# Performance work log

Hardware: AMD Instinct MI355X
Metric: run time of the kernel (lower is better)

Reference implementation:

```python
import jax, jax.numpy as jnp
import numpy as np

B, DIM, C, TOPK = 2, 256, 19, 256
GAMMA = 0.999
HF, WF = 128, 128   # feature spatial res
H, W = 512, 512     # label spatial res
EPS = 1e-12         # F.normalize eps


def setup_inputs() -> dict:
    key = jax.random.key(0)
    k1, k2, k3, k4, k5 = jax.random.split(key, 5)
    features = jax.random.normal(k1, (B, DIM, HF, WF), jnp.float32)
    weight = jax.random.uniform(k2, (B, C, HF, WF), jnp.float32)
    prototypes = jax.random.normal(k3, (C, DIM), jnp.float32)
    update_count = jax.random.randint(k4, (C,), 0, 3).astype(jnp.float32)
    labels = jax.random.randint(k5, (B, H, W), 0, C).astype(jnp.int32)
    return {"features": features, "weight": weight, "prototypes": prototypes,
            "update_count": update_count, "labels": labels}


def _l2norm(x):
    return x / jnp.maximum(jnp.linalg.norm(x, axis=-1, keepdims=True), EPS)


def reference(features, weight, prototypes, update_count, labels):
    # bilinear resize to label resolution (align_corners=False semantics)
    feats = jax.image.resize(features, (B, DIM, H, W), "bilinear")
    wt = jax.image.resize(weight, (B, C, H, W), "bilinear")
    feats = feats.transpose(0, 2, 3, 1).reshape(-1, DIM)   # [N, D]
    wt = wt.transpose(0, 2, 3, 1).reshape(-1, C)           # [N, C]
    lab = labels.reshape(-1)                               # [N]
    valid = lab != 255
    # per-class pixel mask; weights are >=0 (softmax-like), so zeroing
    # out-of-class pixels is equivalent to the torch masked top-k
    cls_mask = valid[:, None] & (lab[:, None] == jnp.arange(C)[None, :])  # [N,C]
    w_cls = jnp.where(cls_mask, wt, 0.0)                   # [N, C]
    topw, topi = jax.lax.top_k(w_cls.T, TOPK)              # [C, K]
    wsum = topw.sum(-1)                                    # [C]
    top_feats = feats[topi]                                # [C, K, D]
    proto = jnp.einsum('ck,ckd->cd', topw, top_feats) / jnp.maximum(wsum, EPS)[:, None]
    proto = _l2norm(proto)                                 # F.normalize before EMA
    has = cls_mask.any(0) & (wsum > 0)                     # class present with nonzero weight
    gamma = jnp.where(update_count == 0, 0.0,
                      jnp.minimum(1.0 - 1.0 / (update_count + 1.0), GAMMA))
    new = gamma[:, None] * prototypes + (1.0 - gamma)[:, None] * proto
    new = jnp.where(has[:, None], new, prototypes)
    new_count = update_count + has.astype(update_count.dtype)
    new = _l2norm(new)                                     # final global normalize
    return new, new_count
```

## Files before the change

kernel.cpp:

```cpp
#include <hip/hip_runtime.h>

#define NB 2
#define NC 19
#define ND 256
#define HFDIM 128
#define SRC_HW 16384
#define HOUT 512
#define NPIX (NB*HOUT*HOUT)
#define KTOP 256
#define NBUCK 16384
#define CAPC 1024
#define CAPE 24
#define NCHUNK 512
#define CHPX 64
#define NBK2 128
#define NDCAP 24
#define NCCAP 24
#define NSLICE 8
#define EPSF 1e-12f

#define AL(x) (((x)+255)&~(size_t)255)
static constexpr size_t OFF_PART  = 0;
static constexpr size_t SZ_PART   = (size_t)NCHUNK*NC*ND*4;
static constexpr size_t OFF_HIST  = 0;
static constexpr size_t OFF_WKEYS = AL(OFF_HIST + (size_t)NC*NBUCK*4);
static constexpr size_t OFF_DLIST = AL(OFF_WKEYS + (size_t)NPIX*4);
static constexpr size_t OFF_CLIST = AL(OFF_DLIST + (size_t)NC*NBK2*NDCAP*8);
static constexpr size_t ALIAS_END = OFF_CLIST + (size_t)NC*NBK2*NCCAP*8;
static_assert(ALIAS_END <= SZ_PART, "alias overflow");
static constexpr size_t OFF_DCNT  = AL(OFF_PART + SZ_PART);
static constexpr size_t OFF_CCNT  = OFF_DCNT + (size_t)NC*NBK2*4;
static constexpr size_t OFF_ECNT  = OFF_CCNT + (size_t)NC*NBK2*4;
static constexpr size_t ZERO_BEG  = OFF_DCNT;
static constexpr size_t ZERO_SZ   = OFF_ECNT + (size_t)NCHUNK*NC*4 - ZERO_BEG;
static constexpr size_t OFF_CUT16 = AL(OFF_ECNT + (size_t)NCHUNK*NC*4);
static constexpr size_t OFF_NHI   = OFF_CUT16 + 256;
static constexpr size_t OFF_CNT   = OFF_NHI   + 256;
static constexpr size_t OFF_WSUM  = OFF_CNT   + 256;
static constexpr size_t OFF_EDATA = AL(OFF_WSUM + 256);
static constexpr size_t OFF_PART2 = AL(OFF_EDATA + (size_t)NCHUNK*NC*CAPE*8);
static constexpr size_t WS_NEED   = OFF_PART2 + (size_t)NSLICE*NC*ND*4;

__device__ __forceinline__ unsigned hperm(unsigned b) { return (b * 5651u) & (NBUCK-1); }

__device__ __forceinline__ void tap1d(int o, int& i0, int& i1, float& f) {
  float pos = (float)o * 0.25f - 0.375f;
  int t0 = (int)floorf(pos);
  float ff = pos - (float)t0;
  int a = t0, b = t0 + 1;
  if (t0 < 0)           { a = 0;       b = 0;       ff = 0.f; }
  else if (b > HFDIM-1) { b = HFDIM-1; ff = 0.f; }
  i0 = a; i1 = b; f = ff;
}

__global__ __launch_bounds__(256) void k_keys(const float* __restrict__ weight,
                                              const int* __restrict__ labels,
                                              float* __restrict__ wkeys,
                                              unsigned* __restrict__ hist) {
  int i4 = blockIdx.x * 256 + threadIdx.x;
  int4 lab = ((const int4*)labels)[i4];
  int n0 = i4 * 4;
  int b = n0 >> 18, y = (n0 >> 9) & 511, x0 = n0 & 511;
  int ya, yb; float fy;
  tap1d(y, ya, yb, fy);
  int labs[4] = {lab.x, lab.y, lab.z, lab.w};
  float wv[4];
  #pragma unroll
  for (int j = 0; j < 4; ++j) {
    int l = labs[j]; float w = 0.f;
    if (l >= 0 && l < NC) {
      int xa, xb; float fx; tap1d(x0 + j, xa, xb, fx);
      const float* pl = weight + (((size_t)(b*NC + l)) << 14);
      float v00 = pl[ya*HFDIM+xa], v10 = pl[yb*HFDIM+xa];
      float v01 = pl[ya*HFDIM+xb], v11 = pl[yb*HFDIM+xb];
      float cA = fmaf(fy, v10, (1.f-fy)*v00);
      float cB = fmaf(fy, v11, (1.f-fy)*v01);
      w = fmaf(fx, cB, (1.f-fx)*cA);
      unsigned bk = __float_as_uint(w) >> 16;
      if (bk > NBUCK-1) bk = NBUCK-1;
      atomicAdd(&hist[l*NBUCK + hperm(bk)], 1u);
    }
    wv[j] = w;
  }
  ((float4*)wkeys)[i4] = make_float4(wv[0], wv[1], wv[2], wv[3]);
}

__global__ __launch_bounds__(256) void k_sel1(const unsigned* __restrict__ hist,
                                              unsigned* __restrict__ cut16,
                                              unsigned* __restrict__ nhi,
                                              unsigned* __restrict__ cnttot) {
  int c = blockIdx.x, t = threadIdx.x;
  __shared__ unsigned sfx[256];
  __shared__ unsigned vals[64];
  __shared__ int sChunk;
  const unsigned* h = hist + (size_t)c * NBUCK;
  unsigned s = 0;
  for (int i = 0; i < 64; ++i) s += h[hperm((unsigned)(t*64 + i))];
  sfx[t] = s;
  if (t == 0) sChunk = -1;
  __syncthreads();
  for (int off = 1; off < 256; off <<= 1) {
    unsigned u = (t + off < 256) ? sfx[t + off] : 0;
    __syncthreads();
    sfx[t] += u;
    __syncthreads();
  }
  unsigned total = sfx[0];
  if (t == 0) cnttot[c] = total;
  unsigned mysfx = sfx[t];
  unsigned nxt = (t < 255) ? sfx[t + 1] : 0;
  if (mysfx >= KTOP && nxt < KTOP) sChunk = t;
  __syncthreads();
  int chunk = sChunk;
  if (chunk < 0) {
    if (t == 0) { cut16[c] = 0; nhi[c] = total - h[hperm(0u)]; }
    return;
  }
  unsigned nAbove = (chunk < 255) ? sfx[chunk + 1] : 0;
  if (t < 64) vals[t] = h[hperm((unsigned)(chunk*64 + t))];
  __syncthreads();
  for (int off = 1; off < 64; off <<= 1) {
    unsigned u = 0;
    if (t < 64) u = (t + off < 64) ? vals[t + off] : 0;
    __syncthreads();
    if (t < 64) vals[t] += u;
    __syncthreads();
  }
  if (t < 64) {
    unsigned sv  = vals[t] + nAbove;
    unsigned svn = (t < 63) ? vals[t + 1] + nAbove : nAbove;
    if (sv >= KTOP && svn < KTOP) { cut16[c] = (unsigned)(chunk*64 + t); nhi[c] = svn; }
  }
}

__global__ __launch_bounds__(256) void k_compact(const int* __restrict__ labels,
                                                 const float* __restrict__ wkeys,
                                                 const unsigned* __restrict__ cut16,
                                                 unsigned* __restrict__ dcnt2, uint2* __restrict__ dlist2,
                                                 unsigned* __restrict__ ccnt2, uint2* __restrict__ clist2) {
  __shared__ unsigned scut[NC], lcnt[NC], lcnt2[NC];
  int t = threadIdx.x, blk = blockIdx.x;
  if (t < NC) { scut[t] = cut16[t]; lcnt[t] = 0; lcnt2[t] = 0; }
  __syncthreads();
  int i4base = blk * 1024;
  for (int it = 0; it < 4; ++it) {
    int i4 = i4base + it*256 + t;
    int4 lab = ((const int4*)labels)[i4];
    float4 wv = ((const float4*)wkeys)[i4];
    int n0 = i4 * 4;
    int labs[4] = {lab.x, lab.y, lab.z, lab.w};
    float ws_[4] = {wv.x, wv.y, wv.z, wv.w};
    #pragma unroll
    for (int j = 0; j < 4; ++j) {
      int l = labs[j]; if (l < 0 || l >= NC) continue;
      unsigned key = __float_as_uint(ws_[j]);
      unsigned pre = key >> 16, cc = scut[l];
      if (pre > cc) {
        unsigned s = atomicAdd(&lcnt[l], 1u);
        if (s < NDCAP) dlist2[((size_t)l*NBK2 + blk)*NDCAP + s] = make_uint2(key, (unsigned)(n0 + j));
      } else if (pre == cc) {
        unsigned s = atomicAdd(&lcnt2[l], 1u);
        if (s < NCCAP) clist2[((size_t)l*NBK2 + blk)*NCCAP + s] = make_uint2(key, (unsigned)(n0 + j));
      }
    }
  }
  __syncthreads();
  if (t < NC) {
    dcnt2[t*NBK2 + blk] = min(lcnt[t],  (unsigned)NDCAP);
    ccnt2[t*NBK2 + blk] = min(lcnt2[t], (unsigned)NCCAP);
  }
}

__device__ __forceinline__ void emit(int c, int sp, float coef,
                                     unsigned* ecnt, uint2* edata) {
  if (coef == 0.f) return;
  int chunk = sp >> 6, pl = sp & 63;
  unsigned s = atomicAdd(&ecnt[chunk*NC + c], 1u);
  if (s < CAPE) edata[((size_t)(chunk*NC + c))*CAPE + s] = make_uint2((unsigned)pl, __float_as_uint(coef));
}

__device__ __forceinline__ void append_taps(int c, unsigned pix, float w,
                                            unsigned* ecnt, uint2* edata) {
  int n = (int)pix; int b = n >> 18, y = (n >> 9) & 511, x = n & 511;
  int ya, yb, xa, xb; float fy, fx;
  tap1d(y, ya, yb, fy); tap1d(x, xa, xb, fx);
  float c00 = (1.f-fy)*(1.f-fx)*w, c01 = (1.f-fy)*fx*w;
  float c10 = fy*(1.f-fx)*w,       c11 = fy*fx*w;
  int base = b * SRC_HW;
  emit(c, base + ya*HFDIM + xa, c00, ecnt, edata);
  emit(c, base + ya*HFDIM + xb, c01, ecnt, edata);
  emit(c, base + yb*HFDIM + xa, c10, ecnt, edata);
  emit(c, base + yb*HFDIM + xb, c11, ecnt, edata);
}

__global__ __launch_bounds__(256) void k_sel3(const uint2* __restrict__ dlist2, const unsigned* __restrict__ dcnt2,
                                              const uint2* __restrict__ clist2, const unsigned* __restrict__ ccnt2,
                                              const unsigned* __restrict__ cut16, const unsigned* __restrict__ nhi,
                                              unsigned* __restrict__ ecnt, uint2* __restrict__ edata,
                                              float* __restrict__ wsum) {
  int c = blockIdx.x, t = threadIdx.x;
  __shared__ uint2 dl[KTOP];
  __shared__ uint2 cand[CAPC];
  __shared__ unsigned ps[256], hh[256];
  __shared__ unsigned sPfx; __shared__ int sNeed; __shared__ unsigned sTie;
  __shared__ float red[256];

  unsigned cnt = (t < NBK2) ? dcnt2[c*NBK2 + t] : 0;
  ps[t] = cnt;
  __syncthreads();
  for (int off = 1; off < 256; off <<= 1) {
    unsigned v = (t >= off) ? ps[t - off] : 0;
    __syncthreads();
    ps[t] += v;
    __syncthreads();
  }
  int dn = (int)ps[255];
  unsigned base = ps[t] - cnt;
  if (t < NBK2) for (unsigned i = 0; i < cnt; ++i) {
    if (base + i < KTOP) dl[base + i] = dlist2[((size_t)c*NBK2 + t)*NDCAP + i];
  }
  __syncthreads();
  unsigned cnt2 = (t < NBK2) ? ccnt2[c*NBK2 + t] : 0;
  ps[t] = cnt2;
  __syncthreads();
  for (int off = 1; off < 256; off <<= 1) {
    unsigned v = (t >= off) ? ps[t - off] : 0;
    __syncthreads();
    ps[t] += v;
    __syncthreads();
  }
  int m = (int)ps[255];
  unsigned base2 = ps[t] - cnt2;
  if (t < NBK2) for (unsigned i = 0; i < cnt2; ++i) {
    if (base2 + i < CAPC) cand[base2 + i] = clist2[((size_t)c*NBK2 + t)*NCCAP + i];
  }
  if (m > CAPC) m = CAPC;
  if (dn > KTOP) dn = KTOP;
  if (t == 0) { sPfx = cut16[c] << 16; sNeed = KTOP - (int)nhi[c]; sTie = 0; }
  __syncthreads();
  for (int rnd = 0; rnd < 2; ++rnd) {
    int sh = rnd ? 0 : 8;
    hh[t] = 0;
    __syncthreads();
    unsigned hiMask = ~((1u << (sh + 8)) - 1u);
    unsigned pfx = sPfx; int need = sNeed;
    for (int k = t; k < m; k += 256) {
      unsigned key = cand[k].x;
      if ((key & hiMask) == (pfx & hiMask)) atomicAdd(&hh[(key >> sh) & 255u], 1u);
    }
    __syncthreads();
    for (int off = 1; off < 256; off <<= 1) {
      unsigned u = (t + off < 256) ? hh[t + off] : 0;
      __syncthreads();
      hh[t] += u;
      __syncthreads();
    }
    unsigned sv = hh[t], svn = (t < 255) ? hh[t + 1] : 0;
    if ((int)sv >= need && (int)svn < need) { sPfx = pfx | ((unsigned)t << sh); sNeed = need - (int)svn; }
    if (t == 0 && (int)hh[0] < need)        { sPfx = pfx; sNeed = need - (int)hh[1]; }
    __syncthreads();
  }
  unsigned cutkey = sPfx;
  int needeq = max(sNeed, 0);
  __syncthreads();
  float wacc = 0.f;
  for (int k = t; k < dn; k += 256) {
    uint2 e = dl[k];
    float w = __uint_as_float(e.x);
    wacc += w;
    append_taps(c, e.y, w, ecnt, edata);
  }
  for (int k = t; k < m; k += 256) {
    uint2 e = cand[k];
    bool sel = e.x > cutkey;
    if (!sel && e.x == cutkey) sel = (atomicAdd(&sTie, 1u) < (unsigned)needeq);
    if (sel) {
      float w = __uint_as_float(e.x);
      wacc += w;
      append_taps(c, e.y, w, ecnt, edata);
    }
  }
  red[t] = wacc; __syncthreads();
  for (int s = 128; s > 0; s >>= 1) { if (t < s) red[t] += red[t + s]; __syncthreads(); }
  if (t == 0) wsum[c] = red[0];
}

__global__ __launch_bounds__(256) void k_contract(const float* __restrict__ feat,
                                                  const unsigned* __restrict__ ecnt,
                                                  const uint2* __restrict__ edata,
                                                  float* __restrict__ part) {
  __shared__ float tile[CHPX * 256];
  int chunk = blockIdx.x, t = threadIdx.x;
  int b = chunk >> 8;
  int p0 = (chunk & 255) << 6;
  const float4* fp = (const float4*)(feat + (((size_t)(b*ND + t)) << 14) + p0);
  #pragma unroll
  for (int i = 0; i < 16; ++i) {
    float4 v = fp[i];
    int p = i * 4;
    tile[(p+0)*256 + t] = v.x; tile[(p+1)*256 + t] = v.y;
    tile[(p+2)*256 + t] = v.z; tile[(p+3)*256 + t] = v.w;
  }
  __syncthreads();
  float* outp = part + ((size_t)chunk * NC) * ND + t;
  #pragma unroll
  for (int c = 0; c < NC; ++c) {
    int n = min((int)ecnt[chunk*NC + c], CAPE);
    const uint2* ed = edata + ((size_t)(chunk*NC + c)) * CAPE;
    float acc = 0.f;
    for (int e = 0; e < n; ++e) {
      uint2 u = ed[e];
      acc = fmaf(__uint_as_float(u.y), tile[u.x*256 + t], acc);
    }
    outp[(size_t)c * ND] = acc;
  }
}

__global__ __launch_bounds__(256) void k_reduce(const float* __restrict__ part,
                                                float* __restrict__ part2) {
  int s = blockIdx.x & (NSLICE-1);
  int c = blockIdx.x / NSLICE;
  int d = threadIdx.x;
  const float* p = part + ((size_t)(s * (NCHUNK/NSLICE)) * NC + c) * ND + d;
  float acc = 0.f;
  #pragma unroll 8
  for (int r = 0; r < NCHUNK/NSLICE; ++r) acc += p[(size_t)r * NC * ND];
  part2[((size_t)s * NC + c) * ND + d] = acc;
}

__global__ __launch_bounds__(256) void k_final(const float* __restrict__ part2,
                                               const float* __restrict__ wsum,
                                               const unsigned* __restrict__ cnttot,
                                               const float* __restrict__ protos,
                                               const float* __restrict__ ucount,
                                               float* __restrict__ out) {
  int c = blockIdx.x, d = threadIdx.x;
  __shared__ float red[256];
  const float* p2 = part2 + (size_t)c * ND + d;
  float psum = 0.f;
  #pragma unroll
  for (int s = 0; s < NSLICE; ++s) psum += p2[(size_t)s * NC * ND];
  float ws = wsum[c];
  float proto = psum / fmaxf(ws, EPSF);
  red[d] = proto * proto;
  __syncthreads();
  for (int s = 128; s > 0; s >>= 1) { if (d < s) red[d] += red[d + s]; __syncthreads(); }
  float norm1 = sqrtf(red[0]);
  __syncthreads();
  float pn = proto / fmaxf(norm1, EPSF);
  float uc = ucount[c];
  float gamma = (uc == 0.f) ? 0.f : fminf(1.f - 1.f / (uc + 1.f), 0.999f);
  bool has = (cnttot[c] > 0u) && (ws > 0.f);
  float oldv = protos[c * ND + d];
  float nv = has ? fmaf(gamma, oldv, (1.f - gamma) * pn) : oldv;
  red[d] = nv * nv;
  __syncthreads();
  for (int s = 128; s > 0; s >>= 1) { if (d < s) red[d] += red[d + s]; __syncthreads(); }
  float norm2 = sqrtf(red[0]);
  out[c * ND + d] = nv / fmaxf(norm2, EPSF);
  if (d == 0) out[NC * ND + c] = uc + (has ? 1.f : 0.f);
}

extern "C" void kernel_launch(void* const* d_in, const int* in_sizes, int n_in,
                              void* d_out, int out_size, void* d_ws, size_t ws_size,
                              hipStream_t stream) {
  const float* feat   = (const float*)d_in[0];
  const float* weight = (const float*)d_in[1];
  const float* protos = (const float*)d_in[2];
  const float* ucount = (const float*)d_in[3];
  const int*   labels = (const int*)d_in[4];
  float* out = (float*)d_out;
  if (ws_size < WS_NEED) return;

  char* ws = (char*)d_ws;
  unsigned* hist   = (unsigned*)(ws + OFF_HIST);
  float*    wkeys  = (float*)   (ws + OFF_WKEYS);
  uint2*    dlist2 = (uint2*)   (ws + OFF_DLIST);
  uint2*    clist2 = (uint2*)   (ws + OFF_CLIST);
  float*    part   = (float*)   (ws + OFF_PART);
  unsigned* dcnt2  = (unsigned*)(ws + OFF_DCNT);
  unsigned* ccnt2  = (unsigned*)(ws + OFF_CCNT);
  unsigned* ecnt   = (unsigned*)(ws + OFF_ECNT);
  unsigned* cut16  = (unsigned*)(ws + OFF_CUT16);
  unsigned* nhiB   = (unsigned*)(ws + OFF_NHI);
  unsigned* cnttot = (unsigned*)(ws + OFF_CNT);
  float*    wsum   = (float*)   (ws + OFF_WSUM);
  uint2*    edata  = (uint2*)   (ws + OFF_EDATA);
  float*    part2  = (float*)   (ws + OFF_PART2);

  hipMemsetAsync(ws + OFF_HIST, 0, (size_t)NC*NBUCK*4, stream);
  hipMemsetAsync(ws + ZERO_BEG, 0, ZERO_SZ, stream);
  k_keys    <<<NPIX/1024, 256, 0, stream>>>(weight, labels, wkeys, hist);
  k_sel1    <<<NC,        256, 0, stream>>>(hist, cut16, nhiB, cnttot);
  k_compact <<<NBK2,      256, 0, stream>>>(labels, wkeys, cut16, dcnt2, dlist2, ccnt2, clist2);
  k_sel3    <<<NC,        256, 0, stream>>>(dlist2, dcnt2, clist2, ccnt2, cut16, nhiB, ecnt, edata, wsum);
  k_contract<<<NCHUNK,    256, 0, stream>>>(feat, ecnt, edata, part);
  k_reduce  <<<NC*NSLICE, 256, 0, stream>>>(part, part2);
  k_final   <<<NC,        256, 0, stream>>>(part2, wsum, cnttot, protos, ucount, out);
}
```

Baseline: 162.8 us.

## Fuse all pipeline stages into one cooperative persistent kernel with grid syncs

Replaces the two memsets and seven separate kernel launches with a single cooperative kernel of 256 blocks. Stages are separated by grid.sync, and shared memory is reused across stages through a union. The aim is to remove per-launch overhead and inter-kernel gaps. In exchange, the grid-wide barriers cost time, the large streaming stages now run on fewer blocks via grid-stride loops, and the 64KB shared union limits occupancy for every stage.

```diff
diff --git a/kernel.cpp b/kernel.cpp
--- a/kernel.cpp
+++ b/kernel.cpp
@@ -1,4 +1,6 @@
 #include <hip/hip_runtime.h>
+#include <hip/hip_cooperative_groups.h>
+namespace cg = cooperative_groups;
 
 #define NB 2
 #define NC 19
@@ -17,6 +19,7 @@
 #define NDCAP 24
 #define NCCAP 24
 #define NSLICE 8
+#define NGRID 256
 #define EPSF 1e-12f
 
 #define AL(x) (((x)+255)&~(size_t)255)
@@ -32,7 +35,7 @@
 static constexpr size_t OFF_CCNT  = OFF_DCNT + (size_t)NC*NBK2*4;
 static constexpr size_t OFF_ECNT  = OFF_CCNT + (size_t)NC*NBK2*4;
 static constexpr size_t ZERO_BEG  = OFF_DCNT;
-static constexpr size_t ZERO_SZ   = OFF_ECNT + (size_t)NCHUNK*NC*4 - ZERO_BEG;
+static constexpr size_t ZCNT      = (2*(size_t)NC*NBK2*4 + (size_t)NCHUNK*NC*4) / 4;
 static constexpr size_t OFF_CUT16 = AL(OFF_ECNT + (size_t)NCHUNK*NC*4);
 static constexpr size_t OFF_NHI   = OFF_CUT16 + 256;
 static constexpr size_t OFF_CNT   = OFF_NHI   + 256;
@@ -51,124 +54,6 @@
   if (t0 < 0)           { a = 0;       b = 0;       ff = 0.f; }
   else if (b > HFDIM-1) { b = HFDIM-1; ff = 0.f; }
   i0 = a; i1 = b; f = ff;
-}
-
-__global__ __launch_bounds__(256) void k_keys(const float* __restrict__ weight,
-                                              const int* __restrict__ labels,
-                                              float* __restrict__ wkeys,
-                                              unsigned* __restrict__ hist) {
-  int i4 = blockIdx.x * 256 + threadIdx.x;
-  int4 lab = ((const int4*)labels)[i4];
-  int n0 = i4 * 4;
-  int b = n0 >> 18, y = (n0 >> 9) & 511, x0 = n0 & 511;
-  int ya, yb; float fy;
-  tap1d(y, ya, yb, fy);
-  int labs[4] = {lab.x, lab.y, lab.z, lab.w};
-  float wv[4];
-  #pragma unroll
-  for (int j = 0; j < 4; ++j) {
-    int l = labs[j]; float w = 0.f;
-    if (l >= 0 && l < NC) {
-      int xa, xb; float fx; tap1d(x0 + j, xa, xb, fx);
-      const float* pl = weight + (((size_t)(b*NC + l)) << 14);
-      float v00 = pl[ya*HFDIM+xa], v10 = pl[yb*HFDIM+xa];
-      float v01 = pl[ya*HFDIM+xb], v11 = pl[yb*HFDIM+xb];
-      float cA = fmaf(fy, v10, (1.f-fy)*v00);
-      float cB = fmaf(fy, v11, (1.f-fy)*v01);
-      w = fmaf(fx, cB, (1.f-fx)*cA);
-      unsigned bk = __float_as_uint(w) >> 16;
-      if (bk > NBUCK-1) bk = NBUCK-1;
-      atomicAdd(&hist[l*NBUCK + hperm(bk)], 1u);
-    }
-    wv[j] = w;
-  }
-  ((float4*)wkeys)[i4] = make_float4(wv[0], wv[1], wv[2], wv[3]);
-}
-
-__global__ __launch_bounds__(256) void k_sel1(const unsigned* __restrict__ hist,
-                                              unsigned* __restrict__ cut16,
-                                              unsigned* __restrict__ nhi,
-                                              unsigned* __restrict__ cnttot) {
-  int c = blockIdx.x, t = threadIdx.x;
-  __shared__ unsigned sfx[256];
-  __shared__ unsigned vals[64];
-  __shared__ int sChunk;
-  const unsigned* h = hist + (size_t)c * NBUCK;
-  unsigned s = 0;
-  for (int i = 0; i < 64; ++i) s += h[hperm((unsigned)(t*64 + i))];
-  sfx[t] = s;
-  if (t == 0) sChunk = -1;
-  __syncthreads();
-  for (int off = 1; off < 256; off <<= 1) {
-    unsigned u = (t + off < 256) ? sfx[t + off] : 0;
-    __syncthreads();
-    sfx[t] += u;
-    __syncthreads();
-  }
-  unsigned total = sfx[0];
-  if (t == 0) cnttot[c] = total;
-  unsigned mysfx = sfx[t];
-  unsigned nxt = (t < 255) ? sfx[t + 1] : 0;
-  if (mysfx >= KTOP && nxt < KTOP) sChunk = t;
-  __syncthreads();
-  int chunk = sChunk;
-  if (chunk < 0) {
-    if (t == 0) { cut16[c] = 0; nhi[c] = total - h[hperm(0u)]; }
-    return;
-  }
-  unsigned nAbove = (chunk < 255) ? sfx[chunk + 1] : 0;
-  if (t < 64) vals[t] = h[hperm((unsigned)(chunk*64 + t))];
-  __syncthreads();
-  for (int off = 1; off < 64; off <<= 1) {
-    unsigned u = 0;
-    if (t < 64) u = (t + off < 64) ? vals[t + off] : 0;
-    __syncthreads();
-    if (t < 64) vals[t] += u;
-    __syncthreads();
-  }
-  if (t < 64) {
-    unsigned sv  = vals[t] + nAbove;
-    unsigned svn = (t < 63) ? vals[t + 1] + nAbove : nAbove;
-    if (sv >= KTOP && svn < KTOP) { cut16[c] = (unsigned)(chunk*64 + t); nhi[c] = svn; }
-  }
-}
-
-__global__ __launch_bounds__(256) void k_compact(const int* __restrict__ labels,
-                                                 const float* __restrict__ wkeys,
-                                                 const unsigned* __restrict__ cut16,
-                                                 unsigned* __restrict__ dcnt2, uint2* __restrict__ dlist2,
-                                                 unsigned* __restrict__ ccnt2, uint2* __restrict__ clist2) {
-  __shared__ unsigned scut[NC], lcnt[NC], lcnt2[NC];
-  int t = threadIdx.x, blk = blockIdx.x;
-  if (t < NC) { scut[t] = cut16[t]; lcnt[t] = 0; lcnt2[t] = 0; }
-  __syncthreads();
-  int i4base = blk * 1024;
-  for (int it = 0; it < 4; ++it) {
-    int i4 = i4base + it*256 + t;
-    int4 lab = ((const int4*)labels)[i4];
-    float4 wv = ((const float4*)wkeys)[i4];
-    int n0 = i4 * 4;
-    int labs[4] = {lab.x, lab.y, lab.z, lab.w};
-    float ws_[4] = {wv.x, wv.y, wv.z, wv.w};
-    #pragma unroll
-    for (int j = 0; j < 4; ++j) {
-      int l = labs[j]; if (l < 0 || l >= NC) continue;
-      unsigned key = __float_as_uint(ws_[j]);
-      unsigned pre = key >> 16, cc = scut[l];
-      if (pre > cc) {
-        unsigned s = atomicAdd(&lcnt[l], 1u);
-        if (s < NDCAP) dlist2[((size_t)l*NBK2 + blk)*NDCAP + s] = make_uint2(key, (unsigned)(n0 + j));
-      } else if (pre == cc) {
-        unsigned s = atomicAdd(&lcnt2[l], 1u);
-        if (s < NCCAP) clist2[((size_t)l*NBK2 + blk)*NCCAP + s] = make_uint2(key, (unsigned)(n0 + j));
-      }
-    }
-  }
-  __syncthreads();
-  if (t < NC) {
-    dcnt2[t*NBK2 + blk] = min(lcnt[t],  (unsigned)NDCAP);
-    ccnt2[t*NBK2 + blk] = min(lcnt2[t], (unsigned)NCCAP);
-  }
 }
 
 __device__ __forceinline__ void emit(int c, int sp, float coef,
@@ -193,172 +78,314 @@
   emit(c, base + yb*HFDIM + xb, c11, ecnt, edata);
 }
 
-__global__ __launch_bounds__(256) void k_sel3(const uint2* __restrict__ dlist2, const unsigned* __restrict__ dcnt2,
-                                              const uint2* __restrict__ clist2, const unsigned* __restrict__ ccnt2,
-                                              const unsigned* __restrict__ cut16, const unsigned* __restrict__ nhi,
-                                              unsigned* __restrict__ ecnt, uint2* __restrict__ edata,
-                                              float* __restrict__ wsum) {
-  int c = blockIdx.x, t = threadIdx.x;
-  __shared__ uint2 dl[KTOP];
-  __shared__ uint2 cand[CAPC];
-  __shared__ unsigned ps[256], hh[256];
-  __shared__ unsigned sPfx; __shared__ int sNeed; __shared__ unsigned sTie;
-  __shared__ float red[256];
-
-  unsigned cnt = (t < NBK2) ? dcnt2[c*NBK2 + t] : 0;
-  ps[t] = cnt;
-  __syncthreads();
-  for (int off = 1; off < 256; off <<= 1) {
-    unsigned v = (t >= off) ? ps[t - off] : 0;
-    __syncthreads();
-    ps[t] += v;
-    __syncthreads();
-  }
-  int dn = (int)ps[255];
-  unsigned base = ps[t] - cnt;
-  if (t < NBK2) for (unsigned i = 0; i < cnt; ++i) {
-    if (base + i < KTOP) dl[base + i] = dlist2[((size_t)c*NBK2 + t)*NDCAP + i];
-  }
-  __syncthreads();
-  unsigned cnt2 = (t < NBK2) ? ccnt2[c*NBK2 + t] : 0;
-  ps[t] = cnt2;
-  __syncthreads();
-  for (int off = 1; off < 256; off <<= 1) {
-    unsigned v = (t >= off) ? ps[t - off] : 0;
-    __syncthreads();
-    ps[t] += v;
-    __syncthreads();
-  }
-  int m = (int)ps[255];
-  unsigned base2 = ps[t] - cnt2;
-  if (t < NBK2) for (unsigned i = 0; i < cnt2; ++i) {
-    if (base2 + i < CAPC) cand[base2 + i] = clist2[((size_t)c*NBK2 + t)*NCCAP + i];
-  }
-  if (m > CAPC) m = CAPC;
-  if (dn > KTOP) dn = KTOP;
-  if (t == 0) { sPfx = cut16[c] << 16; sNeed = KTOP - (int)nhi[c]; sTie = 0; }
-  __syncthreads();
-  for (int rnd = 0; rnd < 2; ++rnd) {
-    int sh = rnd ? 0 : 8;
-    hh[t] = 0;
-    __syncthreads();
-    unsigned hiMask = ~((1u << (sh + 8)) - 1u);
-    unsigned pfx = sPfx; int need = sNeed;
-    for (int k = t; k < m; k += 256) {
-      unsigned key = cand[k].x;
-      if ((key & hiMask) == (pfx & hiMask)) atomicAdd(&hh[(key >> sh) & 255u], 1u);
-    }
-    __syncthreads();
-    for (int off = 1; off < 256; off <<= 1) {
-      unsigned u = (t + off < 256) ? hh[t + off] : 0;
-      __syncthreads();
-      hh[t] += u;
-      __syncthreads();
-    }
-    unsigned sv = hh[t], svn = (t < 255) ? hh[t + 1] : 0;
-    if ((int)sv >= need && (int)svn < need) { sPfx = pfx | ((unsigned)t << sh); sNeed = need - (int)svn; }
-    if (t == 0 && (int)hh[0] < need)        { sPfx = pfx; sNeed = need - (int)hh[1]; }
-    __syncthreads();
-  }
-  unsigned cutkey = sPfx;
-  int needeq = max(sNeed, 0);
-  __syncthreads();
-  float wacc = 0.f;
-  for (int k = t; k < dn; k += 256) {
-    uint2 e = dl[k];
-    float w = __uint_as_float(e.x);
-    wacc += w;
-    append_taps(c, e.y, w, ecnt, edata);
-  }
-  for (int k = t; k < m; k += 256) {
-    uint2 e = cand[k];
-    bool sel = e.x > cutkey;
-    if (!sel && e.x == cutkey) sel = (atomicAdd(&sTie, 1u) < (unsigned)needeq);
-    if (sel) {
-      float w = __uint_as_float(e.x);
-      wacc += w;
-      append_taps(c, e.y, w, ecnt, edata);
-    }
-  }
-  red[t] = wacc; __syncthreads();
-  for (int s = 128; s > 0; s >>= 1) { if (t < s) red[t] += red[t + s]; __syncthreads(); }
-  if (t == 0) wsum[c] = red[0];
-}
-
-__global__ __launch_bounds__(256) void k_contract(const float* __restrict__ feat,
-                                                  const unsigned* __restrict__ ecnt,
-                                                  const uint2* __restrict__ edata,
-                                                  float* __restrict__ part) {
-  __shared__ float tile[CHPX * 256];
-  int chunk = blockIdx.x, t = threadIdx.x;
-  int b = chunk >> 8;
-  int p0 = (chunk & 255) << 6;
-  const float4* fp = (const float4*)(feat + (((size_t)(b*ND + t)) << 14) + p0);
-  #pragma unroll
-  for (int i = 0; i < 16; ++i) {
-    float4 v = fp[i];
-    int p = i * 4;
-    tile[(p+0)*256 + t] = v.x; tile[(p+1)*256 + t] = v.y;
-    tile[(p+2)*256 + t] = v.z; tile[(p+3)*256 + t] = v.w;
-  }
-  __syncthreads();
-  float* outp = part + ((size_t)chunk * NC) * ND + t;
-  #pragma unroll
-  for (int c = 0; c < NC; ++c) {
-    int n = min((int)ecnt[chunk*NC + c], CAPE);
-    const uint2* ed = edata + ((size_t)(chunk*NC + c)) * CAPE;
-    float acc = 0.f;
-    for (int e = 0; e < n; ++e) {
-      uint2 u = ed[e];
-      acc = fmaf(__uint_as_float(u.y), tile[u.x*256 + t], acc);
-    }
-    outp[(size_t)c * ND] = acc;
-  }
-}
-
-__global__ __launch_bounds__(256) void k_reduce(const float* __restrict__ part,
-                                                float* __restrict__ part2) {
-  int s = blockIdx.x & (NSLICE-1);
-  int c = blockIdx.x / NSLICE;
-  int d = threadIdx.x;
-  const float* p = part + ((size_t)(s * (NCHUNK/NSLICE)) * NC + c) * ND + d;
-  float acc = 0.f;
-  #pragma unroll 8
-  for (int r = 0; r < NCHUNK/NSLICE; ++r) acc += p[(size_t)r * NC * ND];
-  part2[((size_t)s * NC + c) * ND + d] = acc;
-}
-
-__global__ __launch_bounds__(256) void k_final(const float* __restrict__ part2,
-                                               const float* __restrict__ wsum,
-                                               const unsigned* __restrict__ cnttot,
+__global__ __launch_bounds__(256) void k_fused(const float* __restrict__ feat,
+                                               const float* __restrict__ weight,
                                                const float* __restrict__ protos,
                                                const float* __restrict__ ucount,
-                                               float* __restrict__ out) {
-  int c = blockIdx.x, d = threadIdx.x;
-  __shared__ float red[256];
-  const float* p2 = part2 + (size_t)c * ND + d;
-  float psum = 0.f;
-  #pragma unroll
-  for (int s = 0; s < NSLICE; ++s) psum += p2[(size_t)s * NC * ND];
-  float ws = wsum[c];
-  float proto = psum / fmaxf(ws, EPSF);
-  red[d] = proto * proto;
-  __syncthreads();
-  for (int s = 128; s > 0; s >>= 1) { if (d < s) red[d] += red[d + s]; __syncthreads(); }
-  float norm1 = sqrtf(red[0]);
-  __syncthreads();
-  float pn = proto / fmaxf(norm1, EPSF);
-  float uc = ucount[c];
-  float gamma = (uc == 0.f) ? 0.f : fminf(1.f - 1.f / (uc + 1.f), 0.999f);
-  bool has = (cnttot[c] > 0u) && (ws > 0.f);
-  float oldv = protos[c * ND + d];
-  float nv = has ? fmaf(gamma, oldv, (1.f - gamma) * pn) : oldv;
-  red[d] = nv * nv;
-  __syncthreads();
-  for (int s = 128; s > 0; s >>= 1) { if (d < s) red[d] += red[d + s]; __syncthreads(); }
-  float norm2 = sqrtf(red[0]);
-  out[c * ND + d] = nv / fmaxf(norm2, EPSF);
-  if (d == 0) out[NC * ND + c] = uc + (has ? 1.f : 0.f);
+                                               const int* __restrict__ labels,
+                                               float* __restrict__ out,
+                                               char* __restrict__ ws) {
+  cg::grid_group grid = cg::this_grid();
+  const int tid = threadIdx.x, bid = blockIdx.x, gdim = gridDim.x;
+  const int gthreads = gdim * 256;
+
+  unsigned* hist   = (unsigned*)(ws + OFF_HIST);
+  float*    wkeys  = (float*)   (ws + OFF_WKEYS);
+  uint2*    dlist2 = (uint2*)   (ws + OFF_DLIST);
+  uint2*    clist2 = (uint2*)   (ws + OFF_CLIST);
+  float*    part   = (float*)   (ws + OFF_PART);
+  unsigned* dcnt2  = (unsigned*)(ws + OFF_DCNT);
+  unsigned* ccnt2  = (unsigned*)(ws + OFF_CCNT);
+  unsigned* ecnt   = (unsigned*)(ws + OFF_ECNT);
+  unsigned* cut16  = (unsigned*)(ws + OFF_CUT16);
+  unsigned* nhi    = (unsigned*)(ws + OFF_NHI);
+  unsigned* cnttot = (unsigned*)(ws + OFF_CNT);
+  float*    wsum   = (float*)   (ws + OFF_WSUM);
+  uint2*    edata  = (uint2*)   (ws + OFF_EDATA);
+  float*    part2  = (float*)   (ws + OFF_PART2);
+
+  __shared__ union {
+    float tile[CHPX * 256];
+    struct { unsigned sfx[256]; unsigned vals[64]; int sChunk; } s1;
+    struct { unsigned scut[NC], lcnt[NC], lcnt2[NC]; } s3;
+    struct {
+      unsigned dlk[KTOP], dlp[KTOP];
+      unsigned ck[CAPC], cp[CAPC];
+      unsigned ps[256], hh[256];
+      unsigned sPfx; int sNeed; unsigned sTie;
+      float red[256];
+    } s4;
+    float redf[256];
+  } sh;
+
+  const int gtid = bid * 256 + tid;
+
+  for (unsigned i = gtid; i < (unsigned)(NC*NBUCK); i += gthreads) hist[i] = 0;
+  {
+    unsigned* zb = (unsigned*)(ws + ZERO_BEG);
+    for (unsigned i = gtid; i < (unsigned)ZCNT; i += gthreads) zb[i] = 0;
+  }
+  grid.sync();
+
+  for (int i4 = gtid; i4 < NPIX/4; i4 += gthreads) {
+    int4 lab = ((const int4*)labels)[i4];
+    int n0 = i4 * 4;
+    int b = n0 >> 18, y = (n0 >> 9) & 511, x0 = n0 & 511;
+    int ya, yb; float fy;
+    tap1d(y, ya, yb, fy);
+    int labs[4] = {lab.x, lab.y, lab.z, lab.w};
+    float wv[4];
+    #pragma unroll
+    for (int j = 0; j < 4; ++j) {
+      int l = labs[j]; float w = 0.f;
+      if (l >= 0 && l < NC) {
+        int xa, xb; float fx; tap1d(x0 + j, xa, xb, fx);
+        const float* pl = weight + (((size_t)(b*NC + l)) << 14);
+        float v00 = pl[ya*HFDIM+xa], v10 = pl[yb*HFDIM+xa];
+        float v01 = pl[ya*HFDIM+xb], v11 = pl[yb*HFDIM+xb];
+        float cA = fmaf(fy, v10, (1.f-fy)*v00);
+        float cB = fmaf(fy, v11, (1.f-fy)*v01);
+        w = fmaf(fx, cB, (1.f-fx)*cA);
+        unsigned bk = __float_as_uint(w) >> 16;
+        if (bk > NBUCK-1) bk = NBUCK-1;
+        atomicAdd(&hist[l*NBUCK + hperm(bk)], 1u);
+      }
+      wv[j] = w;
+    }
+    ((float4*)wkeys)[i4] = make_float4(wv[0], wv[1], wv[2], wv[3]);
+  }
+  grid.sync();
+
+  for (int c = bid; c < NC; c += gdim) {
+    const unsigned* h = hist + (size_t)c * NBUCK;
+    unsigned s = 0;
+    for (int i = 0; i < 64; ++i) s += h[hperm((unsigned)(tid*64 + i))];
+    sh.s1.sfx[tid] = s;
+    if (tid == 0) sh.s1.sChunk = -1;
+    __syncthreads();
+    for (int off = 1; off < 256; off <<= 1) {
+      unsigned u = (tid + off < 256) ? sh.s1.sfx[tid + off] : 0;
+      __syncthreads();
+      sh.s1.sfx[tid] += u;
+      __syncthreads();
+    }
+    unsigned total = sh.s1.sfx[0];
+    if (tid == 0) cnttot[c] = total;
+    unsigned mysfx = sh.s1.sfx[tid];
+    unsigned nxt = (tid < 255) ? sh.s1.sfx[tid + 1] : 0;
+    if (mysfx >= KTOP && nxt < KTOP) sh.s1.sChunk = tid;
+    __syncthreads();
+    int chunk = sh.s1.sChunk;
+    if (chunk < 0) {
+      if (tid == 0) { cut16[c] = 0; nhi[c] = total - h[hperm(0u)]; }
+    } else {
+      unsigned nAbove = (chunk < 255) ? sh.s1.sfx[chunk + 1] : 0;
+      if (tid < 64) sh.s1.vals[tid] = h[hperm((unsigned)(chunk*64 + tid))];
+      __syncthreads();
+      for (int off = 1; off < 64; off <<= 1) {
+        unsigned u = 0;
+        if (tid < 64) u = (tid + off < 64) ? sh.s1.vals[tid + off] : 0;
+        __syncthreads();
+        if (tid < 64) sh.s1.vals[tid] += u;
+        __syncthreads();
+      }
+      if (tid < 64) {
+        unsigned sv  = sh.s1.vals[tid] + nAbove;
+        unsigned svn = (tid < 63) ? sh.s1.vals[tid + 1] + nAbove : nAbove;
+        if (sv >= KTOP && svn < KTOP) { cut16[c] = (unsigned)(chunk*64 + tid); nhi[c] = svn; }
+      }
+    }
+    __syncthreads();
+  }
+  grid.sync();
+
+  for (int blk = bid; blk < NBK2; blk += gdim) {
+    if (tid < NC) { sh.s3.scut[tid] = cut16[tid]; sh.s3.lcnt[tid] = 0; sh.s3.lcnt2[tid] = 0; }
+    __syncthreads();
+    int i4base = blk * 1024;
+    for (int it = 0; it < 4; ++it) {
+      int i4 = i4base + it*256 + tid;
+      int4 lab = ((const int4*)labels)[i4];
+      float4 wv = ((const float4*)wkeys)[i4];
+      int n0 = i4 * 4;
+      int labs[4] = {lab.x, lab.y, lab.z, lab.w};
+      float ws_[4] = {wv.x, wv.y, wv.z, wv.w};
+      #pragma unroll
+      for (int j = 0; j < 4; ++j) {
+        int l = labs[j]; if (l < 0 || l >= NC) continue;
+        unsigned key = __float_as_uint(ws_[j]);
+        unsigned pre = key >> 16, cc = sh.s3.scut[l];
+        if (pre > cc) {
+          unsigned s = atomicAdd(&sh.s3.lcnt[l], 1u);
+          if (s < NDCAP) dlist2[((size_t)l*NBK2 + blk)*NDCAP + s] = make_uint2(key, (unsigned)(n0 + j));
+        } else if (pre == cc) {
+          unsigned s = atomicAdd(&sh.s3.lcnt2[l], 1u);
+          if (s < NCCAP) clist2[((size_t)l*NBK2 + blk)*NCCAP + s] = make_uint2(key, (unsigned)(n0 + j));
+        }
+      }
+    }
+    __syncthreads();
+    if (tid < NC) {
+      dcnt2[tid*NBK2 + blk] = min(sh.s3.lcnt[tid],  (unsigned)NDCAP);
+      ccnt2[tid*NBK2 + blk] = min(sh.s3.lcnt2[tid], (unsigned)NCCAP);
+    }
+    __syncthreads();
+  }
+  grid.sync();
+
+  for (int c = bid; c < NC; c += gdim) {
+    unsigned cnt = (tid < NBK2) ? dcnt2[c*NBK2 + tid] : 0;
+    sh.s4.ps[tid] = cnt;
+    __syncthreads();
+    for (int off = 1; off < 256; off <<= 1) {
+      unsigned v = (tid >= off) ? sh.s4.ps[tid - off] : 0;
+      __syncthreads();
+      sh.s4.ps[tid] += v;
+      __syncthreads();
+    }
+    int dn = (int)sh.s4.ps[255];
+    unsigned base = sh.s4.ps[tid] - cnt;
+    if (tid < NBK2) for (unsigned i = 0; i < cnt; ++i) {
+      if (base + i < KTOP) {
+        uint2 e = dlist2[((size_t)c*NBK2 + tid)*NDCAP + i];
+        sh.s4.dlk[base + i] = e.x; sh.s4.dlp[base + i] = e.y;
+      }
+    }
+    __syncthreads();
+    unsigned cnt2 = (tid < NBK2) ? ccnt2[c*NBK2 + tid] : 0;
+    sh.s4.ps[tid] = cnt2;
+    __syncthreads();
+    for (int off = 1; off < 256; off <<= 1) {
+      unsigned v = (tid >= off) ? sh.s4.ps[tid - off] : 0;
+      __syncthreads();
+      sh.s4.ps[tid] += v;
+      __syncthreads();
+    }
+    int m = (int)sh.s4.ps[255];
+    unsigned base2 = sh.s4.ps[tid] - cnt2;
+    if (tid < NBK2) for (unsigned i = 0; i < cnt2; ++i) {
+      if (base2 + i < CAPC) {
+        uint2 e = clist2[((size_t)c*NBK2 + tid)*NCCAP + i];
+        sh.s4.ck[base2 + i] = e.x; sh.s4.cp[base2 + i] = e.y;
+      }
+    }
+    if (m > CAPC) m = CAPC;
+    if (dn > KTOP) dn = KTOP;
+    if (tid == 0) { sh.s4.sPfx = cut16[c] << 16; sh.s4.sNeed = KTOP - (int)nhi[c]; sh.s4.sTie = 0; }
+    __syncthreads();
+    for (int rnd = 0; rnd < 2; ++rnd) {
+      int shf = rnd ? 0 : 8;
+      sh.s4.hh[tid] = 0;
+      __syncthreads();
+      unsigned hiMask = ~((1u << (shf + 8)) - 1u);
+      unsigned pfx = sh.s4.sPfx; int need = sh.s4.sNeed;
+      for (int k = tid; k < m; k += 256) {
+        unsigned key = sh.s4.ck[k];
+        if ((key & hiMask) == (pfx & hiMask)) atomicAdd(&sh.s4.hh[(key >> shf) & 255u], 1u);
+      }
+      __syncthreads();
+      for (int off = 1; off < 256; off <<= 1) {
+        unsigned u = (tid + off < 256) ? sh.s4.hh[tid + off] : 0;
+        __syncthreads();
+        sh.s4.hh[tid] += u;
+        __syncthreads();
+      }
+      unsigned sv = sh.s4.hh[tid], svn = (tid < 255) ? sh.s4.hh[tid + 1] : 0;
+      if ((int)sv >= need && (int)svn < need) { sh.s4.sPfx = pfx | ((unsigned)tid << shf); sh.s4.sNeed = need - (int)svn; }
+      if (tid == 0 && (int)sh.s4.hh[0] < need)  { sh.s4.sPfx = pfx; sh.s4.sNeed = need - (int)sh.s4.hh[1]; }
+      __syncthreads();
+    }
+    unsigned cutkey = sh.s4.sPfx;
+    int needeq = max(sh.s4.sNeed, 0);
+    __syncthreads();
+    float wacc = 0.f;
+    for (int k = tid; k < dn; k += 256) {
+      float w = __uint_as_float(sh.s4.dlk[k]);
+      wacc += w;
+      append_taps(c, sh.s4.dlp[k], w, ecnt, edata);
+    }
+    for (int k = tid; k < m; k += 256) {
+      unsigned key = sh.s4.ck[k];
+      bool sel = key > cutkey;
+      if (!sel && key == cutkey) sel = (atomicAdd(&sh.s4.sTie, 1u) < (unsigned)needeq);
+      if (sel) {
+        float w = __uint_as_float(key);
+        wacc += w;
+        append_taps(c, sh.s4.cp[k], w, ecnt, edata);
+      }
+    }
+    sh.s4.red[tid] = wacc; __syncthreads();
+    for (int s = 128; s > 0; s >>= 1) { if (tid < s) sh.s4.red[tid] += sh.s4.red[tid + s]; __syncthreads(); }
+    if (tid == 0) wsum[c] = sh.s4.red[0];
+    __syncthreads();
+  }
+  grid.sync();
+
+  for (int chunk = bid; chunk < NCHUNK; chunk += gdim) {
+    int b = chunk >> 8;
+    int p0 = (chunk & 255) << 6;
+    const float4* fp = (const float4*)(feat + (((size_t)(b*ND + tid)) << 14) + p0);
+    #pragma unroll
+    for (int i = 0; i < 16; ++i) {
+      float4 v = fp[i];
+      int p = i * 4;
+      sh.tile[(p+0)*256 + tid] = v.x; sh.tile[(p+1)*256 + tid] = v.y;
+      sh.tile[(p+2)*256 + tid] = v.z; sh.tile[(p+3)*256 + tid] = v.w;
+    }
+    __syncthreads();
+    float* outp = part + ((size_t)chunk * NC) * ND + tid;
+    #pragma unroll
+    for (int c = 0; c < NC; ++c) {
+      int n = min((int)ecnt[chunk*NC + c], CAPE);
+      const uint2* ed = edata + ((size_t)(chunk*NC + c)) * CAPE;
+      float acc = 0.f;
+      for (int e = 0; e < n; ++e) {
+        uint2 u = ed[e];
+        acc = fmaf(__uint_as_float(u.y), sh.tile[u.x*256 + tid], acc);
+      }
+      outp[(size_t)c * ND] = acc;
+    }
+    __syncthreads();
+  }
+  grid.sync();
+
+  for (int w = bid; w < NC*NSLICE; w += gdim) {
+    int s = w & (NSLICE-1);
+    int c = w / NSLICE;
+    const float* p = part + ((size_t)(s * (NCHUNK/NSLICE)) * NC + c) * ND + tid;
+    float acc = 0.f;
+    #pragma unroll 8
+    for (int r = 0; r < NCHUNK/NSLICE; ++r) acc += p[(size_t)r * NC * ND];
+    part2[((size_t)s * NC + c) * ND + tid] = acc;
+  }
+  grid.sync();
+
+  for (int c = bid; c < NC; c += gdim) {
+    const float* p2 = part2 + (size_t)c * ND + tid;
+    float psum = 0.f;
+    #pragma unroll
+    for (int s = 0; s < NSLICE; ++s) psum += p2[(size_t)s * NC * ND];
+    float wsv = wsum[c];
+    float proto = psum / fmaxf(wsv, EPSF);
+    sh.redf[tid] = proto * proto;
+    __syncthreads();
+    for (int s = 128; s > 0; s >>= 1) { if (tid < s) sh.redf[tid] += sh.redf[tid + s]; __syncthreads(); }
+    float norm1 = sqrtf(sh.redf[0]);
+    __syncthreads();
+    float pn = proto / fmaxf(norm1, EPSF);
+    float uc = ucount[c];
+    float gamma = (uc == 0.f) ? 0.f : fminf(1.f - 1.f / (uc + 1.f), 0.999f);
+    bool has = (cnttot[c] > 0u) && (wsv > 0.f);
+    float oldv = protos[c * ND + tid];
+    float nv = has ? fmaf(gamma, oldv, (1.f - gamma) * pn) : oldv;
+    sh.redf[tid] = nv * nv;
+    __syncthreads();
+    for (int s = 128; s > 0; s >>= 1) { if (tid < s) sh.redf[tid] += sh.redf[tid + s]; __syncthreads(); }
+    float norm2 = sqrtf(sh.redf[0]);
+    out[c * ND + tid] = nv / fmaxf(norm2, EPSF);
+    if (tid == 0) out[NC * ND + c] = uc + (has ? 1.f : 0.f);
+    __syncthreads();
+  }
 }
 
 extern "C" void kernel_launch(void* const* d_in, const int* in_sizes, int n_in,
@@ -370,31 +397,10 @@
   const float* ucount = (const float*)d_in[3];
   const int*   labels = (const int*)d_in[4];
   float* out = (float*)d_out;
+  char* wsb = (char*)d_ws;
   if (ws_size < WS_NEED) return;
 
-  char* ws = (char*)d_ws;
-  unsigned* hist   = (unsigned*)(ws + OFF_HIST);
-  float*    wkeys  = (float*)   (ws + OFF_WKEYS);
-  uint2*    dlist2 = (uint2*)   (ws + OFF_DLIST);
-  uint2*    clist2 = (uint2*)   (ws + OFF_CLIST);
-  float*    part   = (float*)   (ws + OFF_PART);
-  unsigned* dcnt2  = (unsigned*)(ws + OFF_DCNT);
-  unsigned* ccnt2  = (unsigned*)(ws + OFF_CCNT);
-  unsigned* ecnt   = (unsigned*)(ws + OFF_ECNT);
-  unsigned* cut16  = (unsigned*)(ws + OFF_CUT16);
-  unsigned* nhiB   = (unsigned*)(ws + OFF_NHI);
-  unsigned* cnttot = (unsigned*)(ws + OFF_CNT);
-  float*    wsum   = (float*)   (ws + OFF_WSUM);
-  uint2*    edata  = (uint2*)   (ws + OFF_EDATA);
-  float*    part2  = (float*)   (ws + OFF_PART2);
-
-  hipMemsetAsync(ws + OFF_HIST, 0, (size_t)NC*NBUCK*4, stream);
-  hipMemsetAsync(ws + ZERO_BEG, 0, ZERO_SZ, stream);
-  k_keys    <<<NPIX/1024, 256, 0, stream>>>(weight, labels, wkeys, hist);
-  k_sel1    <<<NC,        256, 0, stream>>>(hist, cut16, nhiB, cnttot);
-  k_compact <<<NBK2,      256, 0, stream>>>(labels, wkeys, cut16, dcnt2, dlist2, ccnt2, clist2);
-  k_sel3    <<<NC,        256, 0, stream>>>(dlist2, dcnt2, clist2, ccnt2, cut16, nhiB, ecnt, edata, wsum);
-  k_contract<<<NCHUNK,    256, 0, stream>>>(feat, ecnt, edata, part);
-  k_reduce  <<<NC*NSLICE, 256, 0, stream>>>(part, part2);
-  k_final   <<<NC,        256, 0, stream>>>(part2, wsum, cnttot, protos, ucount, out);
+  void* kargs[] = { (void*)&feat, (void*)&weight, (void*)&protos, (void*)&ucount,
+                    (void*)&labels, (void*)&out, (void*)&wsb };
+  hipLaunchCooperativeKernel((void*)k_fused, dim3(NGRID), dim3(256), kargs, 0, stream);
 }
```

Measured after the change: 362.3 us. 123% more time.
